# Kernel optimization log

Hardware: AMD Instinct MI355X
Metric: run time of the kernel (lower is better)

The kernel has to match this reference:

```python
import jax, jax.numpy as jnp
import numpy as np

T = 50        # time_steps_per_action
BATCH = 131072
HID = 100
BETA = 0.9    # snntorch.Leaky beta
THR = 0.5     # snntorch.Leaky threshold


def setup_inputs() -> dict:
    key = jax.random.key(0)
    k_x, k_w1, k_w2 = jax.random.split(key, 3)
    x = jax.random.normal(k_x, (T, BATCH, 2), dtype=jnp.float32)
    # torch.nn.Linear(2, 100, bias=False) weight: [out, in]
    W1 = jax.random.normal(k_w1, (HID, 2), dtype=jnp.float32) * (1.0 / np.sqrt(2))
    W2 = jax.random.normal(k_w2, (2, HID), dtype=jnp.float32) * (1.0 / np.sqrt(HID))
    return {"x": x, "W1": W1, "W2": W2}


def reference(x, W1, W2):
    """LIF two-layer spiking net, scanned over T time steps.
    snntorch Leaky (reset_mechanism='subtract', surrogate_disable):
      mem = beta*mem + input - spk_prev*threshold; spk = (mem > threshold)
    Returns (spk_rec, mem_rec), each [T, batch, 2]."""
    B = x.shape[1]
    dt = x.dtype
    mem1 = jnp.zeros((B, HID), dt)
    spk1 = jnp.zeros((B, HID), dt)
    mem2 = jnp.zeros((B, 2), dt)
    spk2 = jnp.zeros((B, 2), dt)

    def step(carry, x_t):
        mem1, spk1, mem2, spk2 = carry
        cur1 = x_t @ W1.T                                   # [B, HID]
        mem1 = BETA * mem1 + cur1 - spk1 * THR
        spk1 = (mem1 > THR).astype(dt)                      # Heaviside, zero grad
        cur2 = spk1 @ W2.T                                  # [B, 2]
        mem2 = BETA * mem2 + cur2 - spk2 * THR
        spk2 = (mem2 > THR).astype(dt)
        return (mem1, spk1, mem2, spk2), (spk2, mem2)

    _, (spk_rec, mem_rec) = jax.lax.scan(step, (mem1, spk1, mem2, spk2), x)
    return spk_rec, mem_rec
```

## Files before the change

### kernel.cpp

```cpp
#include <hip/hip_runtime.h>

namespace {
constexpr int T_STEPS = 50;
constexpr int BATCH_N = 131072;
constexpr int HIDDEN  = 100;
}

__global__ __launch_bounds__(256)
void snn_fused_kernel(const unsigned int* __restrict__ x_u,
                      const float* __restrict__ W1,
                      const float* __restrict__ W2,
                      unsigned int* __restrict__ out_u)
{
#pragma clang fp contract(off)
    __shared__ float sW1a[HIDDEN], sW1b[HIDDEN], sW20[HIDDEN], sW21[HIDDEN];

    const int tid = threadIdx.x;
    for (int i = tid; i < HIDDEN; i += 256) {
        sW1a[i] = W1[2 * i];
        sW1b[i] = W1[2 * i + 1];
        sW20[i] = W2[i];
        sW21[i] = W2[HIDDEN + i];
    }
    __syncthreads();

    const int b = blockIdx.x * 256 + tid;

    float x0[T_STEPS], x1[T_STEPS];
#pragma unroll
    for (int t = 0; t < T_STEPS; ++t) {
        size_t base = ((size_t)t * BATCH_N + b) * 2;
        x0[t] = __uint_as_float(x_u[base]);
        x1[t] = __uint_as_float(x_u[base + 1]);
    }

    float acc0[T_STEPS], acc1[T_STEPS];
#pragma unroll
    for (int t = 0; t < T_STEPS; ++t) { acc0[t] = 0.0f; acc1[t] = 0.0f; }

#pragma unroll 2
    for (int h = 0; h < HIDDEN; ++h) {
        const float w1a = sW1a[h];
        const float w1b = sW1b[h];
        const float w20 = sW20[h];
        const float w21 = sW21[h];
        float m = 0.0f;
        float s = 0.0f;
#pragma unroll
        for (int t = 0; t < T_STEPS; ++t) {
            float cur = fmaf(x1[t], w1b, x0[t] * w1a);
            m = fmaf(s, -0.5f, fmaf(0.9f, m, cur));
            s = (m > 0.5f) ? 1.0f : 0.0f;
            acc0[t] = fmaf(s, w20, acc0[t]);
            acc1[t] = fmaf(s, w21, acc1[t]);
        }
    }

    const size_t mem_off = (size_t)T_STEPS * BATCH_N * 2;
    float m0 = 0.0f, m1 = 0.0f, s0 = 0.0f, s1 = 0.0f;
#pragma unroll
    for (int t = 0; t < T_STEPS; ++t) {
        m0 = fmaf(s0, -0.5f, fmaf(0.9f, m0, acc0[t]));
        m1 = fmaf(s1, -0.5f, fmaf(0.9f, m1, acc1[t]));
        s0 = (m0 > 0.5f) ? 1.0f : 0.0f;
        s1 = (m1 > 0.5f) ? 1.0f : 0.0f;
        size_t cell = ((size_t)t * BATCH_N + b) * 2;
        out_u[cell]               = __float_as_uint(s0);
        out_u[cell + 1]           = __float_as_uint(s1);
        out_u[mem_off + cell]     = __float_as_uint(m0);
        out_u[mem_off + cell + 1] = __float_as_uint(m1);
    }
}

extern "C" void kernel_launch(void* const* d_in, const int* in_sizes, int n_in,
                              void* d_out, int out_size, void* d_ws, size_t ws_size,
                              hipStream_t stream) {
    int big = 0;
    for (int i = 1; i < n_in; ++i) if (in_sizes[i] > in_sizes[big]) big = i;
    const void* ptrs[3] = {nullptr, nullptr, nullptr};
    int k = 1;
    ptrs[0] = d_in[big];
    for (int i = 0; i < n_in; ++i) {
        if (i == big) continue;
        ptrs[k++] = d_in[i];
    }
    const unsigned int* x_u = (const unsigned int*)ptrs[0];
    const float* W1 = (const float*)ptrs[1];
    const float* W2 = (const float*)ptrs[2];
    unsigned int* out_u = (unsigned int*)d_out;
    dim3 grid(BATCH_N / 256), block(256);
    hipLaunchKernelGGL(snn_fused_kernel, grid, block, 0, stream, x_u, W1, W2, out_u);
}
```

Baseline: 112.3 us.

## Swap loop order to time-outer with per-thread hidden state and interleaved weights

Restructures the kernel so time is the outer loop and 100 hidden membrane potentials live in registers, instead of iterating hidden-outer over 50 preloaded inputs and 100 accumulators. Weights are repacked by a small pre-kernel into an interleaved workspace array and read as uniform (scalar) loads rather than from shared memory. This removes the shared-memory staging and the barrier, and lets output stores stream out per step. The cost is an extra kernel launch and a register footprint that may limit occupancy.

```diff
diff --git a/kernel.cpp b/kernel.cpp
--- a/kernel.cpp
+++ b/kernel.cpp
@@ -6,69 +6,63 @@
 constexpr int HIDDEN  = 100;
 }
 
+__global__ void interleave_weights(const float* __restrict__ W1,
+                                   const float* __restrict__ W2,
+                                   float* __restrict__ wi) {
+    int h = blockIdx.x * 64 + threadIdx.x;
+    if (h < HIDDEN) {
+        wi[4 * h + 0] = W1[2 * h];
+        wi[4 * h + 1] = W1[2 * h + 1];
+        wi[4 * h + 2] = W2[h];
+        wi[4 * h + 3] = W2[HIDDEN + h];
+    }
+}
+
 __global__ __launch_bounds__(256)
-void snn_fused_kernel(const unsigned int* __restrict__ x_u,
-                      const float* __restrict__ W1,
-                      const float* __restrict__ W2,
-                      unsigned int* __restrict__ out_u)
+void snn_touter(const unsigned int* __restrict__ x_u,
+                const float* __restrict__ wi,
+                unsigned int* __restrict__ out_u)
 {
 #pragma clang fp contract(off)
-    __shared__ float sW1a[HIDDEN], sW1b[HIDDEN], sW20[HIDDEN], sW21[HIDDEN];
+    const int b = blockIdx.x * 256 + threadIdx.x;
 
-    const int tid = threadIdx.x;
-    for (int i = tid; i < HIDDEN; i += 256) {
-        sW1a[i] = W1[2 * i];
-        sW1b[i] = W1[2 * i + 1];
-        sW20[i] = W2[i];
-        sW21[i] = W2[HIDDEN + i];
-    }
-    __syncthreads();
+    float m[HIDDEN];
+#pragma unroll
+    for (int h = 0; h < HIDDEN; ++h) m[h] = 0.0f;
 
-    const int b = blockIdx.x * 256 + tid;
+    float m20 = 0.0f, m21 = 0.0f, s20 = 0.0f, s21 = 0.0f;
+    const size_t mem_off = (size_t)T_STEPS * BATCH_N * 2;
 
-    float x0[T_STEPS], x1[T_STEPS];
+    for (int t = 0; t < T_STEPS; ++t) {
+        const size_t cell = ((size_t)t * BATCH_N + b) * 2;
+        const float x0 = __uint_as_float(x_u[cell]);
+        const float x1 = __uint_as_float(x_u[cell + 1]);
+
+        float acc0 = 0.0f, acc1 = 0.0f;
 #pragma unroll
-    for (int t = 0; t < T_STEPS; ++t) {
-        size_t base = ((size_t)t * BATCH_N + b) * 2;
-        x0[t] = __uint_as_float(x_u[base]);
-        x1[t] = __uint_as_float(x_u[base + 1]);
-    }
+        for (int h = 0; h < HIDDEN; ++h) {
+            const float w1a = wi[4 * h + 0];
+            const float w1b = wi[4 * h + 1];
+            const float w20 = wi[4 * h + 2];
+            const float w21 = wi[4 * h + 3];
+            const float cur = fmaf(x1, w1b, x0 * w1a);
+            const float sp  = (m[h] > 0.5f) ? 1.0f : 0.0f;
+            const float mn  = fmaf(sp, -0.5f, fmaf(0.9f, m[h], cur));
+            m[h] = mn;
+            const float sc  = (mn > 0.5f) ? 1.0f : 0.0f;
+            acc0 = fmaf(sc, w20, acc0);
+            acc1 = fmaf(sc, w21, acc1);
+        }
 
-    float acc0[T_STEPS], acc1[T_STEPS];
-#pragma unroll
-    for (int t = 0; t < T_STEPS; ++t) { acc0[t] = 0.0f; acc1[t] = 0.0f; }
+        m20 = fmaf(s20, -0.5f, fmaf(0.9f, m20, acc0));
+        m21 = fmaf(s21, -0.5f, fmaf(0.9f, m21, acc1));
+        s20 = (m20 > 0.5f) ? 1.0f : 0.0f;
+        s21 = (m21 > 0.5f) ? 1.0f : 0.0f;
 
-#pragma unroll 2
-    for (int h = 0; h < HIDDEN; ++h) {
-        const float w1a = sW1a[h];
-        const float w1b = sW1b[h];
-        const float w20 = sW20[h];
-        const float w21 = sW21[h];
-        float m = 0.0f;
-        float s = 0.0f;
-#pragma unroll
-        for (int t = 0; t < T_STEPS; ++t) {
-            float cur = fmaf(x1[t], w1b, x0[t] * w1a);
-            m = fmaf(s, -0.5f, fmaf(0.9f, m, cur));
-            s = (m > 0.5f) ? 1.0f : 0.0f;
-            acc0[t] = fmaf(s, w20, acc0[t]);
-            acc1[t] = fmaf(s, w21, acc1[t]);
-        }
-    }
-
-    const size_t mem_off = (size_t)T_STEPS * BATCH_N * 2;
-    float m0 = 0.0f, m1 = 0.0f, s0 = 0.0f, s1 = 0.0f;
-#pragma unroll
-    for (int t = 0; t < T_STEPS; ++t) {
-        m0 = fmaf(s0, -0.5f, fmaf(0.9f, m0, acc0[t]));
-        m1 = fmaf(s1, -0.5f, fmaf(0.9f, m1, acc1[t]));
-        s0 = (m0 > 0.5f) ? 1.0f : 0.0f;
-        s1 = (m1 > 0.5f) ? 1.0f : 0.0f;
-        size_t cell = ((size_t)t * BATCH_N + b) * 2;
-        out_u[cell]               = __float_as_uint(s0);
-        out_u[cell + 1]           = __float_as_uint(s1);
-        out_u[mem_off + cell]     = __float_as_uint(m0);
-        out_u[mem_off + cell + 1] = __float_as_uint(m1);
+        out_u[cell]               = __float_as_uint(s20);
+        out_u[cell + 1]           = __float_as_uint(s21);
+        out_u[mem_off + cell]     = __float_as_uint(m20);
+        out_u[mem_off + cell + 1] = __float_as_uint(m21);
     }
 }
 
@@ -87,7 +81,11 @@
     const unsigned int* x_u = (const unsigned int*)ptrs[0];
     const float* W1 = (const float*)ptrs[1];
     const float* W2 = (const float*)ptrs[2];
+    float* wi = (float*)d_ws;
     unsigned int* out_u = (unsigned int*)d_out;
-    dim3 grid(BATCH_N / 256), block(256);
-    hipLaunchKernelGGL(snn_fused_kernel, grid, block, 0, stream, x_u, W1, W2, out_u);
+
+    hipLaunchKernelGGL(interleave_weights, dim3(2), dim3(64), 0, stream,
+                       W1, W2, wi);
+    hipLaunchKernelGGL(snn_touter, dim3(BATCH_N / 256), dim3(256), 0, stream,
+                       x_u, wi, out_u);
 }
```

Result: slower. 230.8 us (+105.6%).
